# Kernel optimization log

Measured on AMD Instinct MI355X. Metric: run time of the kernel, lower is better.

## Reference

```python
import jax, jax.numpy as jnp
import numpy as np

B, S = 4, 1024          # 4 prefill sequences of length 1024 (cu_seqlens equal-length)
D_MODEL = 2048
N_HEADS = 32
N_KV_HEADS = 8
HEAD_DIM = D_MODEL // N_HEADS          # 64
GROUPS = N_HEADS // N_KV_HEADS         # 4
ROPE_THETA = 10000.0
SCALE = HEAD_DIM ** -0.5


def setup_inputs() -> dict:
    key = jax.random.key(0)
    ks = jax.random.split(key, 6)
    T = B * S
    hidden_states = jax.random.normal(ks[0], (T, D_MODEL), jnp.float32)
    # rotary tables: positions restart per sequence (prefill)
    pos = jnp.tile(jnp.arange(S, dtype=jnp.float32), B)            # [T]
    inv_freq = 1.0 / (ROPE_THETA ** (jnp.arange(0, HEAD_DIM, 2, dtype=jnp.float32) / HEAD_DIM))
    freqs = pos[:, None] * inv_freq[None, :]                        # [T, HEAD_DIM/2]
    cos, sin = jnp.cos(freqs), jnp.sin(freqs)
    std = D_MODEL ** -0.5
    Wq = jax.random.normal(ks[1], (D_MODEL, N_HEADS * HEAD_DIM), jnp.float32) * std
    Wk = jax.random.normal(ks[2], (D_MODEL, N_KV_HEADS * HEAD_DIM), jnp.float32) * std
    Wv = jax.random.normal(ks[3], (D_MODEL, N_KV_HEADS * HEAD_DIM), jnp.float32) * std
    Wo = jax.random.normal(ks[4], (N_HEADS * HEAD_DIM, D_MODEL), jnp.float32) * std
    return {"hidden_states": hidden_states, "cos": cos, "sin": sin,
            "Wq": Wq, "Wk": Wk, "Wv": Wv, "Wo": Wo}


def _rope(x, cos, sin):
    # NeoX-style rotary: x [T, H, D], cos/sin [T, D/2]
    half = x.shape[-1] // 2
    x1, x2 = x[..., :half], x[..., half:]
    c, s = cos[:, None, :], sin[:, None, :]
    return jnp.concatenate([x1 * c - x2 * s, x2 * c + x1 * s], axis=-1)


def reference(hidden_states, cos, sin, Wq, Wk, Wv, Wo):
    T = hidden_states.shape[0]
    q = (hidden_states @ Wq).reshape(T, N_HEADS, HEAD_DIM)
    k = (hidden_states @ Wk).reshape(T, N_KV_HEADS, HEAD_DIM)
    v = (hidden_states @ Wv).reshape(T, N_KV_HEADS, HEAD_DIM)
    q = _rope(q, cos, sin)
    k = _rope(k, cos, sin)
    # equal-length varlen prefill -> [B, S, H, D]
    q = q.reshape(B, S, N_HEADS, HEAD_DIM)
    k = jnp.repeat(k.reshape(B, S, N_KV_HEADS, HEAD_DIM), GROUPS, axis=2)  # GQA expand
    v = jnp.repeat(v.reshape(B, S, N_KV_HEADS, HEAD_DIM), GROUPS, axis=2)
    scores = jnp.einsum("bqhd,bkhd->bhqk", q, k) * SCALE
    causal = jnp.tril(jnp.ones((S, S), dtype=bool))
    scores = jnp.where(causal[None, None], scores, jnp.finfo(scores.dtype).min)
    probs = jax.nn.softmax(scores, axis=-1)
    attn = jnp.einsum("bhqk,bkhd->bqhd", probs, v).reshape(T, N_HEADS * HEAD_DIM)
    return attn @ Wo
```

## Files before the change

### kernel.cpp

```cpp
#include <hip/hip_runtime.h>
#include <type_traits>


typedef __bf16 bf16x8 __attribute__((ext_vector_type(8)));
typedef __bf16 bf16x4 __attribute__((ext_vector_type(4)));
typedef float f32x4 __attribute__((ext_vector_type(4)));
typedef unsigned short u16;
typedef unsigned int u32;

#define DEVI __device__ __forceinline__

DEVI u16 f2bf(float f) {
  u32 u = __builtin_bit_cast(u32, f);
  u += 0x7FFF + ((u >> 16) & 1);
  return (u16)(u >> 16);
}

DEVI void ld16_lds(const void* g, void* l) {
  __builtin_amdgcn_global_load_lds((const __attribute__((address_space(1))) u32*)g,
                                   (__attribute__((address_space(3))) u32*)l, 16, 0, 0);
}

__global__ __launch_bounds__(256) void convert_f32_bf16(const float* __restrict__ src,
                                                        u16* __restrict__ dst, int n4) {
  int i = blockIdx.x * 256 + threadIdx.x;
  if (i >= n4) return;
  float4 v = ((const float4*)src)[i];
  ushort4 o;
  o.x = f2bf(v.x); o.y = f2bf(v.y); o.z = f2bf(v.z); o.w = f2bf(v.w);
  ((ushort4*)dst)[i] = o;
}

__global__ __launch_bounds__(256) void trans_f32_bf16(const float* __restrict__ src,
                                                      u16* __restrict__ dst, int R, int C,
                                                      float scale) {
  __shared__ float tile[32][33];
  int c0 = blockIdx.x * 32, r0 = blockIdx.y * 32;
  int tx = threadIdx.x & 31, ty = threadIdx.x >> 5;
#pragma unroll
  for (int i = 0; i < 32; i += 8)
    tile[ty + i][tx] = src[(size_t)(r0 + ty + i) * C + (c0 + tx)];
  __syncthreads();
#pragma unroll
  for (int i = 0; i < 32; i += 8)
    dst[(size_t)(c0 + ty + i) * R + (r0 + tx)] = f2bf(tile[tx][ty + i] * scale);
}

template <typename OutT, bool ROPE>
__global__ __launch_bounds__(256) void gemm_bt(const u16* __restrict__ A, const u16* __restrict__ BT,
                                               OutT* __restrict__ C, int M, int N, int K,
                                               const float* __restrict__ cs,
                                               const float* __restrict__ sn) {
  __shared__ u16 As[128 * 64];
  __shared__ u16 Bs[128 * 64];
  const int tid = threadIdx.x;
  const int lane = tid & 63, wave = tid >> 6;
  const int quad = lane >> 4, l16 = lane & 15;
  const int m0 = blockIdx.y * 128, n0 = blockIdx.x * 128;
  const int wr = (wave >> 1) * 64, wc = (wave & 1) * 64;

  f32x4 acc[4][4] = {};

  const int srow = tid >> 3;
  const int sc = (tid & 7) ^ (srow & 7);
  const u16* Ag = A + (size_t)(m0 + srow) * K + sc * 8;
  const u16* Bg = BT + (size_t)(n0 + srow) * K + sc * 8;

  for (int k0 = 0; k0 < K; k0 += 64) {
    __syncthreads();
#pragma unroll
    for (int i = 0; i < 4; i++) {
      ld16_lds(Ag + k0 + (size_t)i * 32 * K, &As[tid * 8 + i * 2048]);
      ld16_lds(Bg + k0 + (size_t)i * 32 * K, &Bs[tid * 8 + i * 2048]);
    }
    __syncthreads();

#pragma unroll
    for (int s = 0; s < 2; s++) {
      bf16x8 af[4], bfr[4];
#pragma unroll
      for (int i = 0; i < 4; i++) {
        int ar = wr + i * 16 + l16;
        af[i] = *(const bf16x8*)&As[ar * 64 + (((s * 4 + quad) ^ (ar & 7)) * 8)];
        int br = wc + i * 16 + l16;
        bfr[i] = *(const bf16x8*)&Bs[br * 64 + (((s * 4 + quad) ^ (br & 7)) * 8)];
      }
#pragma unroll
      for (int i = 0; i < 4; i++)
#pragma unroll
        for (int j = 0; j < 4; j++)
          acc[i][j] = __builtin_amdgcn_mfma_f32_16x16x32_bf16(af[i], bfr[j], acc[i][j], 0, 0, 0);
    }
  }

  if constexpr (ROPE) {
    if (n0 + wc < 2560) {
#pragma unroll
      for (int i = 0; i < 4; i++) {
        int t0 = m0 + wr + i * 16 + quad * 4;
#pragma unroll
        for (int jj = 0; jj < 2; jj++) {
          int d = jj * 16 + l16;
#pragma unroll
          for (int r = 0; r < 4; r++) {
            float c = cs[(size_t)(t0 + r) * 32 + d];
            float s = sn[(size_t)(t0 + r) * 32 + d];
            float x1 = acc[i][jj][r], x2 = acc[i][jj + 2][r];
            acc[i][jj][r] = x1 * c - x2 * s;
            acc[i][jj + 2][r] = x2 * c + x1 * s;
          }
        }
      }
    }
  }

#pragma unroll
  for (int i = 0; i < 4; i++) {
    int row = m0 + wr + i * 16 + quad * 4;
#pragma unroll
    for (int j = 0; j < 4; j++) {
      int col = n0 + wc + j * 16 + l16;
#pragma unroll
      for (int r = 0; r < 4; r++) {
        size_t off = (size_t)(row + r) * N + col;
        if constexpr (sizeof(OutT) == 2) C[off] = f2bf(acc[i][j][r]);
        else C[off] = acc[i][j][r];
      }
    }
  }
}

__global__ __launch_bounds__(256) void vkt_build(const u16* __restrict__ qkv,
                                                 u16* __restrict__ vkt) {
  __shared__ u16 Vn[128 * 64];
  const int kt = blockIdx.x, kvh = blockIdx.y, b = blockIdx.z;
  const int tid = threadIdx.x;
  const u16* src = qkv + ((size_t)b * 1024 + kt * 128) * 3072 + 2560 + kvh * 64;
  {
    int tok = tid >> 1, hf = tid & 1;
    const uint4* s4 = (const uint4*)(src + (size_t)tok * 3072 + hf * 32);
    uint4* d4 = (uint4*)&Vn[tok * 64 + hf * 32];
#pragma unroll
    for (int j = 0; j < 4; j++) d4[j] = s4[j];
  }
  __syncthreads();
  u16* img = vkt + ((((size_t)b * 8 + kvh) * 8 + kt) << 13);
#pragma unroll
  for (int i = 0; i < 4; i++) {
    int c = tid * 4 + i;
    int dd = c >> 4, chsw = c & 15;
    int ch = chsw ^ (dd & 15);
    u16 tmp[8];
#pragma unroll
    for (int p = 0; p < 8; p++) {
      int col = ch * 8 + p;
      int g = col >> 5, kl = col & 31;
      int kph = ((kl >> 2) & 1) * 16 + ((kl >> 4) & 1) * 8 + ((kl >> 3) & 1) * 4 + (kl & 3);
      tmp[p] = Vn[(g * 32 + kph) * 64 + dd];
    }
    *(uint4*)&img[c * 8] = *(const uint4*)tmp;
  }
}

__global__ __launch_bounds__(256, 2) void flash_attn(const u16* __restrict__ qkv,
                                                     const u16* __restrict__ vkt,
                                                     u16* __restrict__ attn) {
  __shared__ u16 Ks[2][128 * 64];
  __shared__ u16 VT[2][64 * 128];

  const int tid = threadIdx.x;
  const int lane = tid & 63, wave = tid >> 6;
  const int quad = lane >> 4, l16 = lane & 15;
  const int qtA = blockIdx.x, qtB = 7 - blockIdx.x;
  const int h = blockIdx.y, b = blockIdx.z, kvh = h >> 2;
  const size_t tokBase = (size_t)b * 1024;
  const int qcol = h * 64, kcol = 2048 + kvh * 64;
  const int srow = tid >> 3, spc = tid & 7, ssc = spc ^ (srow & 7);

  auto stageK = [&](const u16* gbase, u16* L) {
#pragma unroll
    for (int i = 0; i < 4; i++)
      ld16_lds(gbase + (size_t)(srow + i * 32) * 3072 + ssc * 8, &L[tid * 8 + i * 2048]);
  };
  const u16* vimg = vkt + (((size_t)b * 8 + kvh) << 16);
  auto stageV = [&](int kt, u16* L) {
    const u16* g = vimg + ((size_t)kt << 13);
#pragma unroll
    for (int i = 0; i < 4; i++)
      ld16_lds(g + i * 2048 + tid * 8, &L[tid * 8 + i * 2048]);
  };

  stageK(qkv + (tokBase + qtA * 128) * 3072 + qcol, Ks[0]);
  stageK(qkv + (tokBase + qtB * 128) * 3072 + qcol, Ks[1]);
  __syncthreads();
  bf16x8 qfA[2][2], qfB[2][2];
#pragma unroll
  for (int nq = 0; nq < 2; nq++) {
    int qrow = wave * 32 + nq * 16 + l16;
#pragma unroll
    for (int ks = 0; ks < 2; ks++) {
      int c = (ks * 4 + quad) ^ (qrow & 7);
      qfA[nq][ks] = *(const bf16x8*)&Ks[0][qrow * 64 + c * 8];
      qfB[nq][ks] = *(const bf16x8*)&Ks[1][qrow * 64 + c * 8];
    }
  }
  __syncthreads();

  float lA[2] = {0.f, 0.f}, lB[2] = {0.f, 0.f};
  f32x4 oA[4][2] = {}, oB[4][2] = {};

  auto proc = [&](const bf16x8 (&kf)[2][2], const bf16x8 (&va)[4], const bf16x8 (&qf)[2][2],
                  f32x4 (&o)[4][2], float (&lacc)[2], bool msk, int c) {
    f32x4 s[2][2] = {};
#pragma unroll
    for (int mkl = 0; mkl < 2; mkl++)
#pragma unroll
      for (int ks = 0; ks < 2; ks++) {
        s[0][mkl] = __builtin_amdgcn_mfma_f32_16x16x32_bf16(kf[mkl][ks], qf[0][ks], s[0][mkl], 0, 0, 0);
        s[1][mkl] = __builtin_amdgcn_mfma_f32_16x16x32_bf16(kf[mkl][ks], qf[1][ks], s[1][mkl], 0, 0, 0);
      }
    if (msk) {
#pragma unroll
      for (int nq = 0; nq < 2; nq++) {
        int q = wave * 32 + nq * 16 + l16;
#pragma unroll
        for (int mkl = 0; mkl < 2; mkl++)
#pragma unroll
          for (int r = 0; r < 4; r++)
            if ((c * 2 + mkl) * 16 + quad * 4 + r > q) s[nq][mkl][r] = -3e38f;
      }
    }
    bf16x8 pf[2];
#pragma unroll
    for (int nq = 0; nq < 2; nq++) {
      float a0 = 0.f;
#pragma unroll
      for (int mkl = 0; mkl < 2; mkl++)
#pragma unroll
        for (int r = 0; r < 4; r++) {
          float p = __builtin_amdgcn_exp2f(s[nq][mkl][r]);
          s[nq][mkl][r] = p;
          a0 += p;
        }
      lacc[nq] += a0;
      pf[nq][0] = (__bf16)s[nq][0][0]; pf[nq][1] = (__bf16)s[nq][0][1];
      pf[nq][2] = (__bf16)s[nq][0][2]; pf[nq][3] = (__bf16)s[nq][0][3];
      pf[nq][4] = (__bf16)s[nq][1][0]; pf[nq][5] = (__bf16)s[nq][1][1];
      pf[nq][6] = (__bf16)s[nq][1][2]; pf[nq][7] = (__bf16)s[nq][1][3];
    }
#pragma unroll
    for (int md = 0; md < 4; md++) {
      o[md][0] = __builtin_amdgcn_mfma_f32_16x16x32_bf16(va[md], pf[0], o[md][0], 0, 0, 0);
      o[md][1] = __builtin_amdgcn_mfma_f32_16x16x32_bf16(va[md], pf[1], o[md][1], 0, 0, 0);
    }
  };

  stageK(qkv + tokBase * 3072 + kcol, Ks[0]);
  stageV(0, VT[0]);

  for (int kt = 0; kt <= qtB; kt++) {
    const int cur = kt & 1;
    __syncthreads();
    if (kt < qtB) {
      stageK(qkv + (tokBase + (kt + 1) * 128) * 3072 + kcol, Ks[1 - cur]);
      stageV(kt + 1, VT[1 - cur]);
    }
    const bool doA = (kt <= qtA), mA = (kt == qtA), mB = (kt == qtB);
    const u16* K = Ks[cur];
    const u16* V = VT[cur];
#pragma unroll
    for (int c = 0; c < 4; c++) {
      bf16x8 kf[2][2];
#pragma unroll
      for (int mkl = 0; mkl < 2; mkl++) {
        int krow = (c * 2 + mkl) * 16 + l16;
#pragma unroll
        for (int ks = 0; ks < 2; ks++)
          kf[mkl][ks] = *(const bf16x8*)&K[krow * 64 + ((ks * 4 + quad) ^ (krow & 7)) * 8];
      }
      bf16x8 va[4];
#pragma unroll
      for (int md = 0; md < 4; md++) {
        int dd = md * 16 + l16;
        va[md] = *(const bf16x8*)&V[dd * 128 + ((c * 4 + quad) ^ l16) * 8];
      }
      proc(kf, va, qfB, oB, lB, mB, c);
      if (doA) proc(kf, va, qfA, oA, lA, mA, c);
    }
  }

  auto epilogue = [&](const f32x4 (&o)[4][2], const float (&lacc)[2], int qt_tile) {
#pragma unroll
    for (int nq = 0; nq < 2; nq++) {
      float l = lacc[nq];
      l += __shfl_xor(l, 16);
      l += __shfl_xor(l, 32);
      float inv = 1.0f / l;
      int t = qt_tile * 128 + wave * 32 + nq * 16 + l16;
      size_t rowOff = (tokBase + t) * 2048 + qcol;
#pragma unroll
      for (int md = 0; md < 4; md++) {
        bf16x4 w;
        w[0] = (__bf16)(o[md][nq][0] * inv);
        w[1] = (__bf16)(o[md][nq][1] * inv);
        w[2] = (__bf16)(o[md][nq][2] * inv);
        w[3] = (__bf16)(o[md][nq][3] * inv);
        *(bf16x4*)&attn[rowOff + md * 16 + quad * 4] = w;
      }
    }
  };
  epilogue(oB, lB, qtB);
  epilogue(oA, lA, qtA);
}

extern "C" void kernel_launch(void* const* d_in, const int* in_sizes, int n_in,
                              void* d_out, int out_size, void* d_ws, size_t ws_size,
                              hipStream_t stream) {
  const float* hs = (const float*)d_in[0];
  const float* cs = (const float*)d_in[1];
  const float* sn = (const float*)d_in[2];
  const float* Wq = (const float*)d_in[3];
  const float* Wk = (const float*)d_in[4];
  const float* Wv = (const float*)d_in[5];
  const float* Wo = (const float*)d_in[6];
  float* out = (float*)d_out;

  char* ws = (char*)d_ws;
  u16* hsB   = (u16*)(ws);
  u16* vkt   = (u16*)(ws);
  u16* wqkvT = (u16*)(ws + 16777216);
  u16* woT   = (u16*)(ws + 29360128);
  u16* qkv   = (u16*)(ws + 37748736);
  u16* attnB = (u16*)(ws + 62914560);

  const float QSCALE = 0.18033688011112042f;

  convert_f32_bf16<<<8192, 256, 0, stream>>>(hs, hsB, 4096 * 2048 / 4);
  trans_f32_bf16<<<dim3(64, 64), 256, 0, stream>>>(Wq, wqkvT, 2048, 2048, QSCALE);
  trans_f32_bf16<<<dim3(16, 64), 256, 0, stream>>>(Wk, wqkvT + (size_t)2048 * 2048, 2048, 512, 1.0f);
  trans_f32_bf16<<<dim3(16, 64), 256, 0, stream>>>(Wv, wqkvT + (size_t)2560 * 2048, 2048, 512, 1.0f);
  trans_f32_bf16<<<dim3(64, 64), 256, 0, stream>>>(Wo, woT, 2048, 2048, 1.0f);

  gemm_bt<u16, true><<<dim3(24, 32), 256, 0, stream>>>(hsB, wqkvT, qkv, 4096, 3072, 2048, cs, sn);
  vkt_build<<<dim3(8, 8, 4), 256, 0, stream>>>(qkv, vkt);
  flash_attn<<<dim3(4, 32, 4), 256, 0, stream>>>(qkv, vkt, attnB);
  gemm_bt<float, false><<<dim3(16, 32), 256, 0, stream>>>(attnB, woT, out, 4096, 2048, 2048,
                                                          nullptr, nullptr);
}
```

Measured before the change: 285.1 us.

## Double-buffer LDS and enlarge GEMM tiles to 256-row blocks with 512 threads

The bf16 GEMM kernel is templated on tile geometry and moves to 512-thread blocks. The QKV projection uses 256x256 tiles and the output projection uses 256x128 tiles. LDS staging is now double-buffered: the next K-tile's global-to-LDS loads are issued before the current tile's MFMAs, which removes one barrier per iteration. MFMA sections are also wrapped in s_setprio. The aim is to overlap memory with compute and raise reuse per block. In exchange, LDS use is much larger, which limits occupancy, and the QKV launch has only 192 blocks, fewer than the CU count.

```diff
diff --git a/kernel.cpp b/kernel.cpp
--- a/kernel.cpp
+++ b/kernel.cpp
@@ -46,68 +46,96 @@
     dst[(size_t)(c0 + ty + i) * R + (r0 + tx)] = f2bf(tile[tx][ty + i] * scale);
 }
 
-template <typename OutT, bool ROPE>
-__global__ __launch_bounds__(256) void gemm_bt(const u16* __restrict__ A, const u16* __restrict__ BT,
-                                               OutT* __restrict__ C, int M, int N, int K,
-                                               const float* __restrict__ cs,
-                                               const float* __restrict__ sn) {
-  __shared__ u16 As[128 * 64];
-  __shared__ u16 Bs[128 * 64];
+template <typename OutT, bool ROPE, int BN, int GM, int GN, int WM, int WN>
+__global__ __launch_bounds__(512, 2) void gemm_bt(const u16* __restrict__ A,
+                                                  const u16* __restrict__ BT,
+                                                  OutT* __restrict__ C, int M, int N, int K,
+                                                  const float* __restrict__ cs,
+                                                  const float* __restrict__ sn) {
+  static_assert(GM * GN == 8 && 16 * WM * GM == 256 && 16 * WN * GN == BN, "geom");
+  __shared__ u16 As[2][256 * 64];
+  __shared__ u16 Bs[2][BN * 64];
   const int tid = threadIdx.x;
   const int lane = tid & 63, wave = tid >> 6;
   const int quad = lane >> 4, l16 = lane & 15;
-  const int m0 = blockIdx.y * 128, n0 = blockIdx.x * 128;
-  const int wr = (wave >> 1) * 64, wc = (wave & 1) * 64;
-
-  f32x4 acc[4][4] = {};
-
-  const int srow = tid >> 3;
-  const int sc = (tid & 7) ^ (srow & 7);
-  const u16* Ag = A + (size_t)(m0 + srow) * K + sc * 8;
-  const u16* Bg = BT + (size_t)(n0 + srow) * K + sc * 8;
-
-  for (int k0 = 0; k0 < K; k0 += 64) {
+  const int m0 = blockIdx.y * 256, n0 = blockIdx.x * BN;
+  const int wr = wave / GN, wc = wave % GN;
+
+  f32x4 acc[WM][WN] = {};
+
+  auto stageTile = [&](int t, int bufIdx) {
+    const int k0 = t * 64;
+    u16* Ad = &As[bufIdx][0];
+    u16* Bd = &Bs[bufIdx][0];
+#pragma unroll
+    for (int i = 0; i < 4; ++i) {
+      int id = i * 512 + tid;
+      int row = id >> 3, ch = id & 7;
+      int sch = ch ^ (row & 7);
+      ld16_lds(A + (size_t)(m0 + row) * K + k0 + sch * 8, Ad + id * 8);
+    }
+#pragma unroll
+    for (int i = 0; i < BN / 64; ++i) {
+      int id = i * 512 + tid;
+      int row = id >> 3, ch = id & 7;
+      int sch = ch ^ (row & 7);
+      ld16_lds(BT + (size_t)(n0 + row) * K + k0 + sch * 8, Bd + id * 8);
+    }
+  };
+
+  const int NT = K / 64;
+  stageTile(0, 0);
+  __syncthreads();
+
+  for (int t = 0; t < NT; ++t) {
+    const int c = t & 1;
+    if (t + 1 < NT) stageTile(t + 1, 1 - c);
+    const u16* Ab = &As[c][0];
+    const u16* Bb = &Bs[c][0];
+#pragma unroll
+    for (int ks = 0; ks < 2; ++ks) {
+      bf16x8 bfv[WN];
+#pragma unroll
+      for (int j = 0; j < WN; ++j) {
+        int rb = wc * (16 * WN) + j * 16 + l16;
+        bfv[j] = *(const bf16x8*)&Bb[rb * 64 + (((ks * 4 + quad) ^ (rb & 7)) * 8)];
+      }
+#pragma unroll
+      for (int mh = 0; mh < WM / 4; ++mh) {
+        bf16x8 af[4];
+#pragma unroll
+        for (int i = 0; i < 4; ++i) {
+          int r = wr * (16 * WM) + (mh * 4 + i) * 16 + l16;
+          af[i] = *(const bf16x8*)&Ab[r * 64 + (((ks * 4 + quad) ^ (r & 7)) * 8)];
+        }
+        __builtin_amdgcn_s_setprio(1);
+#pragma unroll
+        for (int i = 0; i < 4; ++i)
+#pragma unroll
+          for (int j = 0; j < WN; ++j)
+            acc[mh * 4 + i][j] =
+                __builtin_amdgcn_mfma_f32_16x16x32_bf16(af[i], bfv[j], acc[mh * 4 + i][j], 0, 0, 0);
+        __builtin_amdgcn_s_setprio(0);
+      }
+    }
     __syncthreads();
-#pragma unroll
-    for (int i = 0; i < 4; i++) {
-      ld16_lds(Ag + k0 + (size_t)i * 32 * K, &As[tid * 8 + i * 2048]);
-      ld16_lds(Bg + k0 + (size_t)i * 32 * K, &Bs[tid * 8 + i * 2048]);
-    }
-    __syncthreads();
-
-#pragma unroll
-    for (int s = 0; s < 2; s++) {
-      bf16x8 af[4], bfr[4];
-#pragma unroll
-      for (int i = 0; i < 4; i++) {
-        int ar = wr + i * 16 + l16;
-        af[i] = *(const bf16x8*)&As[ar * 64 + (((s * 4 + quad) ^ (ar & 7)) * 8)];
-        int br = wc + i * 16 + l16;
-        bfr[i] = *(const bf16x8*)&Bs[br * 64 + (((s * 4 + quad) ^ (br & 7)) * 8)];
-      }
-#pragma unroll
-      for (int i = 0; i < 4; i++)
-#pragma unroll
-        for (int j = 0; j < 4; j++)
-          acc[i][j] = __builtin_amdgcn_mfma_f32_16x16x32_bf16(af[i], bfr[j], acc[i][j], 0, 0, 0);
-    }
   }
 
   if constexpr (ROPE) {
-    if (n0 + wc < 2560) {
-#pragma unroll
-      for (int i = 0; i < 4; i++) {
-        int t0 = m0 + wr + i * 16 + quad * 4;
+    if (n0 + wc * (16 * WN) < 2560) {
+#pragma unroll
+      for (int i = 0; i < WM; i++) {
+        int t0 = m0 + wr * (16 * WM) + i * 16 + quad * 4;
 #pragma unroll
         for (int jj = 0; jj < 2; jj++) {
           int d = jj * 16 + l16;
 #pragma unroll
           for (int r = 0; r < 4; r++) {
-            float c = cs[(size_t)(t0 + r) * 32 + d];
-            float s = sn[(size_t)(t0 + r) * 32 + d];
+            float cv = cs[(size_t)(t0 + r) * 32 + d];
+            float sv = sn[(size_t)(t0 + r) * 32 + d];
             float x1 = acc[i][jj][r], x2 = acc[i][jj + 2][r];
-            acc[i][jj][r] = x1 * c - x2 * s;
-            acc[i][jj + 2][r] = x2 * c + x1 * s;
+            acc[i][jj][r] = x1 * cv - x2 * sv;
+            acc[i][jj + 2][r] = x2 * cv + x1 * sv;
           }
         }
       }
@@ -115,11 +143,11 @@
   }
 
 #pragma unroll
-  for (int i = 0; i < 4; i++) {
-    int row = m0 + wr + i * 16 + quad * 4;
-#pragma unroll
-    for (int j = 0; j < 4; j++) {
-      int col = n0 + wc + j * 16 + l16;
+  for (int i = 0; i < WM; i++) {
+    int row = m0 + wr * (16 * WM) + i * 16 + quad * 4;
+#pragma unroll
+    for (int j = 0; j < WN; j++) {
+      int col = n0 + wc * (16 * WN) + j * 16 + l16;
 #pragma unroll
       for (int r = 0; r < 4; r++) {
         size_t off = (size_t)(row + r) * N + col;
@@ -341,9 +369,10 @@
   trans_f32_bf16<<<dim3(16, 64), 256, 0, stream>>>(Wv, wqkvT + (size_t)2560 * 2048, 2048, 512, 1.0f);
   trans_f32_bf16<<<dim3(64, 64), 256, 0, stream>>>(Wo, woT, 2048, 2048, 1.0f);
 
-  gemm_bt<u16, true><<<dim3(24, 32), 256, 0, stream>>>(hsB, wqkvT, qkv, 4096, 3072, 2048, cs, sn);
+  gemm_bt<u16, true, 256, 2, 4, 8, 4><<<dim3(12, 16), 512, 0, stream>>>(
+      hsB, wqkvT, qkv, 4096, 3072, 2048, cs, sn);
   vkt_build<<<dim3(8, 8, 4), 256, 0, stream>>>(qkv, vkt);
   flash_attn<<<dim3(4, 32, 4), 256, 0, stream>>>(qkv, vkt, attnB);
-  gemm_bt<float, false><<<dim3(16, 32), 256, 0, stream>>>(attnB, woT, out, 4096, 2048, 2048,
-                                                          nullptr, nullptr);
-}
+  gemm_bt<float, false, 128, 4, 2, 4, 4><<<dim3(16, 16), 512, 0, stream>>>(
+      attnB, woT, out, 4096, 2048, 2048, nullptr, nullptr);
+}
```

Result: no change. 281.8 us (-1.1%).
